# Kernel optimization log

Hardware: AMD Instinct MI355X
Metric: run time of the kernel (lower is better)

Reference implementation:

```python
import jax, jax.numpy as jnp
import numpy as np

N, E = 50000, 1600000
F_IN, EDGE_DIM, HID, HEADS, NCLS = 64, 16, 128, 4, 40
C = HID // HEADS  # per-head dim = 32


def setup_inputs() -> dict:
    key = jax.random.key(0)
    ks = jax.random.split(key, 20)
    s = 0.1
    inp = {
        'x': jax.random.normal(ks[0], (N, F_IN), jnp.float32),
        'edge_index': jax.random.randint(ks[1], (2, E), 0, N, jnp.int64),
        'edge_attr': jax.random.normal(ks[2], (E, EDGE_DIM), jnp.float32),
        # layer 1 params
        'W1': jax.random.normal(ks[3], (HID, F_IN), jnp.float32) * s,
        'as1': jax.random.normal(ks[4], (HEADS, C), jnp.float32) * s,
        'ad1': jax.random.normal(ks[5], (HEADS, C), jnp.float32) * s,
        'ae1': jax.random.normal(ks[6], (HEADS, C), jnp.float32) * s,
        'We1': jax.random.normal(ks[7], (HID, EDGE_DIM), jnp.float32) * s,
        'b1': jnp.zeros((HID,), jnp.float32),
        # layer 2 params
        'W2': jax.random.normal(ks[8], (HID, HID), jnp.float32) * s,
        'as2': jax.random.normal(ks[9], (HEADS, C), jnp.float32) * s,
        'ad2': jax.random.normal(ks[10], (HEADS, C), jnp.float32) * s,
        'ae2': jax.random.normal(ks[11], (HEADS, C), jnp.float32) * s,
        'We2': jax.random.normal(ks[12], (HID, EDGE_DIM), jnp.float32) * s,
        'b2': jnp.zeros((HID,), jnp.float32),
        # final classifier
        'Wlin': jax.random.normal(ks[13], (NCLS, HID), jnp.float32) * s,
        'blin': jnp.zeros((NCLS,), jnp.float32),
    }
    return inp


def gat_conv(x, src, dst, eattr, W, a_s, a_d, a_e, We, b):
    """PyG GATConv (concat=True, add_self_loops=True, fill_value='mean'), eval mode."""
    n = x.shape[0]
    H, Cd = a_s.shape
    h = (x @ W.T).reshape(n, H, Cd)  # [N,H,C]
    # self-loop edge_attr = per-destination mean of incoming edge_attr
    cnt = jax.ops.segment_sum(jnp.ones((dst.shape[0],), eattr.dtype), dst, num_segments=n)
    mean_ea = jax.ops.segment_sum(eattr, dst, num_segments=n) / jnp.maximum(cnt, 1.0)[:, None]
    loops = jnp.arange(n, dtype=src.dtype)
    s_idx = jnp.concatenate([src, loops])
    d_idx = jnp.concatenate([dst, loops])
    ea = jnp.concatenate([eattr, mean_ea], axis=0)  # [E+N, edge_dim]
    e = (ea @ We.T).reshape(-1, H, Cd)
    # edge-wise attention logits
    alpha = (h * a_s).sum(-1)[s_idx] + (h * a_d).sum(-1)[d_idx] + (e * a_e).sum(-1)  # [E+N,H]
    alpha = jax.nn.leaky_relu(alpha, 0.2)
    # segment softmax over destination neighborhoods (every node has a self-loop)
    amax = jax.ops.segment_max(alpha, d_idx, num_segments=n)
    ex = jnp.exp(alpha - amax[d_idx])
    den = jax.ops.segment_sum(ex, d_idx, num_segments=n)
    coef = ex / (den[d_idx] + 1e-16)
    out = jax.ops.segment_sum(h[s_idx] * coef[:, :, None], d_idx, num_segments=n)
    return out.reshape(n, H * Cd) + b


def reference(x, edge_index, edge_attr, W1, as1, ad1, ae1, We1, b1,
              W2, as2, ad2, ae2, We2, b2, Wlin, blin):
    src, dst = edge_index[0], edge_index[1]
    h = jax.nn.relu(gat_conv(x, src, dst, edge_attr, W1, as1, ad1, ae1, We1, b1))
    h = jax.nn.relu(gat_conv(h, src, dst, edge_attr, W2, as2, ad2, ae2, We2, b2))
    logits = h @ Wlin.T + blin
    return jax.nn.log_softmax(logits, axis=1)
```

## Files before the change

kernel.cpp:

```cpp
#include <hip/hip_runtime.h>
#include <hip/hip_bf16.h>
#include <math.h>


#define CHUNK 2048

typedef __attribute__((ext_vector_type(8))) short short8;
typedef __attribute__((ext_vector_type(4))) float floatx4;
typedef __attribute__((ext_vector_type(2))) float floatx2;

__device__ __forceinline__ unsigned short f2bf(float f) {
  unsigned u = __float_as_uint(f);
  unsigned r = u + 0x7FFFu + ((u >> 16) & 1u);
  return (unsigned short)(r >> 16);
}
__device__ __forceinline__ float bf2f(unsigned short b) {
  return __uint_as_float(((unsigned)b) << 16);
}

__global__ __launch_bounds__(128) void wa_kernel(const float* __restrict__ ae1,
                                                 const float* __restrict__ We1,
                                                 const float* __restrict__ ae2,
                                                 const float* __restrict__ We2,
                                                 float* __restrict__ Wa) {
  int t = threadIdx.x;
  const float* ae = (t < 64) ? ae1 : ae2;
  const float* We = (t < 64) ? We1 : We2;
  int h = (t >> 4) & 3;
  int d = t & 15;
  float s = 0.f;
  for (int c = 0; c < 32; ++c) s += ae[h * 32 + c] * We[(h * 32 + c) * 16 + d];
  Wa[t] = s;
}

__global__ __launch_bounds__(256) void alphaseq_kernel(const float* __restrict__ ea,
                                                       const float* __restrict__ Wa,
                                                       uint2* __restrict__ tA1,
                                                       uint2* __restrict__ tA2, int E) {
  __shared__ float wa[128];
  if (threadIdx.x < 128) wa[threadIdx.x] = Wa[threadIdx.x];
  __syncthreads();
  int e = blockIdx.x * 256 + threadIdx.x;
  if (e >= E) return;
  const float4* p = (const float4*)(ea + (size_t)e * 16);
  float4 q0 = p[0], q1 = p[1], q2 = p[2], q3 = p[3];
  float v[16] = {q0.x, q0.y, q0.z, q0.w, q1.x, q1.y, q1.z, q1.w,
                 q2.x, q2.y, q2.z, q2.w, q3.x, q3.y, q3.z, q3.w};
  unsigned short rr[8];
#pragma unroll
  for (int h = 0; h < 8; ++h) {
    float s = 0.f;
#pragma unroll
    for (int d = 0; d < 16; ++d) s += v[d] * wa[h * 16 + d];
    rr[h] = f2bf(s);
  }
  uint2 lo, hi;
  lo.x = ((unsigned)rr[1] << 16) | rr[0];
  lo.y = ((unsigned)rr[3] << 16) | rr[2];
  hi.x = ((unsigned)rr[5] << 16) | rr[4];
  hi.y = ((unsigned)rr[7] << 16) | rr[6];
  tA1[e] = lo;
  tA2[e] = hi;
}

__global__ __launch_bounds__(512) void hist_kernel(const int* __restrict__ dst,
                                                   int* __restrict__ bucketCnt,
                                                   int E, int NB) {
  __shared__ int hist[512];
  const int tid = threadIdx.x;
  hist[tid] = 0;
  __syncthreads();
  const int e0 = blockIdx.x * CHUNK, e1 = min(e0 + CHUNK, E);
  for (int e = e0 + tid; e < e1; e += 512) atomicAdd(&hist[dst[e] >> 7], 1);
  __syncthreads();
  if (tid < NB && hist[tid]) atomicAdd(&bucketCnt[tid], hist[tid]);
}

__global__ __launch_bounds__(512) void scanB_kernel(const int* __restrict__ bucketCnt,
                                                    int* __restrict__ bucketOffs,
                                                    int* __restrict__ bucketPos,
                                                    int* __restrict__ offs,
                                                    int NB, int N, int E) {
  __shared__ int sc[512];
  const int tid = threadIdx.x;
  const int v = (tid < NB) ? bucketCnt[tid] : 0;
  sc[tid] = v;
  __syncthreads();
  for (int off = 1; off < 512; off <<= 1) {
    int t = (tid >= off) ? sc[tid - off] : 0;
    __syncthreads();
    sc[tid] += t;
    __syncthreads();
  }
  const int excl = sc[tid] - v;
  if (tid < NB) { bucketOffs[tid] = excl; bucketPos[tid] = excl; }
  if (tid == 0) { bucketOffs[NB] = E; offs[N] = E; }
}

__global__ __launch_bounds__(512) void partB_kernel(const int* __restrict__ src,
                                                    const int* __restrict__ dst,
                                                    const uint2* __restrict__ tA1,
                                                    const uint2* __restrict__ tA2,
                                                    int* __restrict__ bucketPos,
                                                    int4* __restrict__ binned16,
                                                    int* __restrict__ binned4,
                                                    unsigned char* __restrict__ dlArr,
                                                    int E, int NB) {
  __shared__ int hist[512], sc[512], lbase[513], gbase[512], lcnt[512];
  __shared__ int4 stg16[CHUNK];
  __shared__ int stg4[CHUNK];
  __shared__ unsigned char stg1[CHUNK];
  const int tid = threadIdx.x;
  const int e0 = blockIdx.x * CHUNK;
  const int e1 = min(e0 + CHUNK, E);
  hist[tid] = 0; lcnt[tid] = 0;
  __syncthreads();
  for (int e = e0 + tid; e < e1; e += 512) atomicAdd(&hist[dst[e] >> 7], 1);
  __syncthreads();
  sc[tid] = hist[tid];
  __syncthreads();
  for (int off = 1; off < 512; off <<= 1) {
    int t = (tid >= off) ? sc[tid - off] : 0;
    __syncthreads();
    sc[tid] += t;
    __syncthreads();
  }
  lbase[tid + 1] = sc[tid];
  if (tid == 0) lbase[0] = 0;
  if (tid < NB && hist[tid] > 0) gbase[tid] = atomicAdd(&bucketPos[tid], hist[tid]);
  __syncthreads();
  for (int e = e0 + tid; e < e1; e += 512) {
    const int d = dst[e];
    const int b = d >> 7;
    const int lr = atomicAdd(&lcnt[b], 1);
    const uint2 a1 = tA1[e];
    const uint2 a2 = tA2[e];
    int4 v;
    v.x = (src[e] & 0xFFFF) | ((d & 127) << 16);
    v.y = (int)a1.x;
    v.z = (int)a1.y;
    v.w = (int)a2.x;
    const int sp = lbase[b] + lr;
    stg16[sp] = v;
    stg4[sp] = (int)a2.y;
    stg1[sp] = (unsigned char)(d & 127);
  }
  __syncthreads();
  const int total = e1 - e0;
  for (int t = tid; t < total; t += 512) {
    int lo = 0, hi = 511;
    while (lo < hi) {
      int mid = (lo + hi + 1) >> 1;
      if (lbase[mid] <= t) lo = mid; else hi = mid - 1;
    }
    const int g = gbase[lo] + (t - lbase[lo]);
    binned16[g] = stg16[t];
    binned4[g] = stg4[t];
    dlArr[g] = stg1[t];
  }
}

__global__ __launch_bounds__(256) void passC_kernel(const int4* __restrict__ binned16,
                                                    const int* __restrict__ binned4,
                                                    const unsigned char* __restrict__ dlArr,
                                                    const int* __restrict__ bucketOffs,
                                                    int* __restrict__ srcS,
                                                    uint2* __restrict__ aeS1,
                                                    uint2* __restrict__ aeS2,
                                                    int* __restrict__ offs, int N) {
  __shared__ int cnt[128], dbase[129], dpos[128];
  const int tid = threadIdx.x;
  const int b = blockIdx.x;
  const int bo = bucketOffs[b], be = bucketOffs[b + 1];
  const int m = be - bo;
  if (tid < 128) { cnt[tid] = 0; dpos[tid] = 0; }
  __syncthreads();
  for (int t = tid; t < m; t += 256) atomicAdd(&cnt[dlArr[bo + t]], 1);
  __syncthreads();
  for (int off = 1; off < 128; off <<= 1) {
    int t = (tid < 128 && tid >= (unsigned)off) ? cnt[tid - off] : 0;
    __syncthreads();
    if (tid < 128) cnt[tid] += t;
    __syncthreads();
  }
  if (tid == 0) dbase[0] = 0;
  if (tid < 128) dbase[tid + 1] = cnt[tid];
  __syncthreads();
  const int dcnt = min(128, N - (b << 7));
  if (tid < dcnt) offs[(b << 7) + tid] = bo + dbase[tid];
  for (int t = tid; t < m; t += 256) {
    const int4 v = binned16[bo + t];
    const int w4 = binned4[bo + t];
    const int dl = (v.x >> 16) & 127;
    const int p = dbase[dl] + atomicAdd(&dpos[dl], 1);
    srcS[bo + p] = v.x & 0xFFFF;
    aeS1[bo + p] = make_uint2((unsigned)v.y, (unsigned)v.z);
    aeS2[bo + p] = make_uint2((unsigned)v.w, (unsigned)w4);
  }
}

__global__ __launch_bounds__(256) void cvt2_kernel(const float* __restrict__ a,
                                                   unsigned short* __restrict__ ao, int na,
                                                   const float* __restrict__ b,
                                                   unsigned short* __restrict__ bo, int nb) {
  int i = blockIdx.x * 256 + threadIdx.x;
  if (i < na) ao[i] = f2bf(a[i]);
  else if (i < na + nb) bo[i - na] = f2bf(b[i - na]);
}

__global__ __launch_bounds__(256) void cvtw_kernel(const float* __restrict__ Wlin,
                                                   unsigned short* __restrict__ whi,
                                                   unsigned short* __restrict__ wlo) {
  int i = blockIdx.x * 256 + threadIdx.x;
  if (i >= 48 * 128) return;
  float v = (i < 40 * 128) ? Wlin[i] : 0.f;
  unsigned short h = f2bf(v);
  whi[i] = h;
  wlo[i] = f2bf(v - bf2f(h));
}

__global__ __launch_bounds__(256) void gemm_mfma_f32_kernel(const float* __restrict__ X,
                                                            const unsigned short* __restrict__ Wb,
                                                            unsigned short* __restrict__ H,
                                                            int n) {
  const int w = threadIdx.x >> 6;
  const int lane = threadIdx.x & 63;
  const int m0 = blockIdx.x * 64;
  const int quad = lane >> 4;
  const int l15 = lane & 15;
  floatx4 acc[4][2];
#pragma unroll
  for (int mt = 0; mt < 4; ++mt)
#pragma unroll
    for (int nt = 0; nt < 2; ++nt) acc[mt][nt] = (floatx4)(0.f);

  int rowm[4];
#pragma unroll
  for (int mt = 0; mt < 4; ++mt) {
    int r = m0 + mt * 16 + l15;
    rowm[mt] = (r < n) ? r : (n - 1);
  }
  const int ncol0 = (w << 5) + l15;

#pragma unroll
  for (int kc = 0; kc < 64; kc += 32) {
    const int koff = kc + (quad << 3);
    short8 a[4], b[2];
#pragma unroll
    for (int mt = 0; mt < 4; ++mt) {
      const float* pr = X + (size_t)rowm[mt] * 64 + koff;
      float4 q0 = *(const float4*)pr;
      float4 q1 = *(const float4*)(pr + 4);
      a[mt][0] = (short)f2bf(q0.x); a[mt][1] = (short)f2bf(q0.y);
      a[mt][2] = (short)f2bf(q0.z); a[mt][3] = (short)f2bf(q0.w);
      a[mt][4] = (short)f2bf(q1.x); a[mt][5] = (short)f2bf(q1.y);
      a[mt][6] = (short)f2bf(q1.z); a[mt][7] = (short)f2bf(q1.w);
    }
#pragma unroll
    for (int nt = 0; nt < 2; ++nt)
      b[nt] = *(const short8*)(Wb + (size_t)(ncol0 + nt * 16) * 64 + koff);
#pragma unroll
    for (int mt = 0; mt < 4; ++mt)
#pragma unroll
      for (int nt = 0; nt < 2; ++nt)
        acc[mt][nt] = __builtin_amdgcn_mfma_f32_16x16x32_bf16(a[mt], b[nt], acc[mt][nt], 0, 0, 0);
  }
#pragma unroll
  for (int mt = 0; mt < 4; ++mt) {
    const int rbase = m0 + mt * 16 + (quad << 2);
#pragma unroll
    for (int nt = 0; nt < 2; ++nt) {
      const int col = ncol0 + nt * 16;
#pragma unroll
      for (int r = 0; r < 4; ++r) {
        const int row = rbase + r;
        if (row < n) H[(size_t)row * 128 + col] = f2bf(acc[mt][nt][r]);
      }
    }
  }
}

__global__ __launch_bounds__(256) void gemm_mfma_kernel(const unsigned short* __restrict__ X,
                                                        const unsigned short* __restrict__ Wb,
                                                        unsigned short* __restrict__ H,
                                                        int n, int K) {
  const int w = threadIdx.x >> 6;
  const int lane = threadIdx.x & 63;
  const int m0 = blockIdx.x * 64;
  const int quad = lane >> 4;
  const int l15 = lane & 15;
  floatx4 acc[4][2];
#pragma unroll
  for (int mt = 0; mt < 4; ++mt)
#pragma unroll
    for (int nt = 0; nt < 2; ++nt) acc[mt][nt] = (floatx4)(0.f);

  int rowm[4];
#pragma unroll
  for (int mt = 0; mt < 4; ++mt) {
    int r = m0 + mt * 16 + l15;
    rowm[mt] = (r < n) ? r : (n - 1);
  }
  const int ncol0 = (w << 5) + l15;

  for (int kc = 0; kc < K; kc += 32) {
    const int koff = kc + (quad << 3);
    short8 a[4], b[2];
#pragma unroll
    for (int mt = 0; mt < 4; ++mt)
      a[mt] = *(const short8*)(X + (size_t)rowm[mt] * K + koff);
#pragma unroll
    for (int nt = 0; nt < 2; ++nt)
      b[nt] = *(const short8*)(Wb + (size_t)(ncol0 + nt * 16) * K + koff);
#pragma unroll
    for (int mt = 0; mt < 4; ++mt)
#pragma unroll
      for (int nt = 0; nt < 2; ++nt)
        acc[mt][nt] = __builtin_amdgcn_mfma_f32_16x16x32_bf16(a[mt], b[nt], acc[mt][nt], 0, 0, 0);
  }
#pragma unroll
  for (int mt = 0; mt < 4; ++mt) {
    const int rbase = m0 + mt * 16 + (quad << 2);
#pragma unroll
    for (int nt = 0; nt < 2; ++nt) {
      const int col = ncol0 + nt * 16;
#pragma unroll
      for (int r = 0; r < 4; ++r) {
        const int row = rbase + r;
        if (row < n) H[(size_t)row * 128 + col] = f2bf(acc[mt][nt][r]);
      }
    }
  }
}

__global__ __launch_bounds__(256) void score_kernel(const unsigned short* __restrict__ h,
                                                    const float* __restrict__ a_s,
                                                    const float* __restrict__ a_d,
                                                    float* __restrict__ ssc,
                                                    float* __restrict__ dsc, int n) {
  int gid = blockIdx.x * 256 + threadIdx.x;
  int node = gid >> 6;
  int lane = threadIdx.x & 63;
  if (node >= n) return;
  int ch = lane * 2;
  ushort2 hq = *(const ushort2*)(h + (size_t)node * 128 + ch);
  float h0 = bf2f(hq.x), h1 = bf2f(hq.y);
  float ps = h0 * a_s[ch] + h1 * a_s[ch + 1];
  float pd = h0 * a_d[ch] + h1 * a_d[ch + 1];
#pragma unroll
  for (int off = 8; off; off >>= 1) {
    ps += __shfl_xor(ps, off, 16);
    pd += __shfl_xor(pd, off, 16);
  }
  if ((lane & 15) == 0) {
    int head = lane >> 4;
    ssc[node * 4 + head] = ps;
    dsc[node * 4 + head] = pd;
  }
}

__device__ __forceinline__ float leaky02(float a) { return a > 0.f ? a : 0.2f * a; }
__device__ __forceinline__ float sel4(float4 v, int h) {
  return (h == 0) ? v.x : (h == 1) ? v.y : (h == 2) ? v.z : v.w;
}

__global__ __launch_bounds__(256) void agg_kernel(const unsigned short* __restrict__ hin,
                                                  const float* __restrict__ ssc,
                                                  const float* __restrict__ dsc,
                                                  const unsigned short* __restrict__ aeS,
                                                  const int* __restrict__ offs,
                                                  const int* __restrict__ srcS,
                                                  const float* __restrict__ bias,
                                                  unsigned short* __restrict__ hout, int n) {
  __shared__ int sbuf[4][64];
  __shared__ float pbuf[4][256];
  const int tid = threadIdx.x;
  const int wv = tid >> 6;
  const int lane = tid & 63;
  const int node = blockIdx.x * 4 + wv;
  if (node >= n) return;
  const int l32 = lane & 31;
  const int half = lane >> 5;
  const int ch4 = l32 * 4;
  const int headB = l32 >> 3;
  const float4 dv = *(const float4*)(dsc + (size_t)node * 4);
  float4 l4 = make_float4(0.f, 0.f, 0.f, 0.f);
  float4 sa = make_float4(0.f, 0.f, 0.f, 0.f);
  floatx2 acc01 = (floatx2)(0.f);
  floatx2 acc23 = (floatx2)(0.f);
  const int j0 = offs[node], j1 = offs[node + 1];

  for (int jc = j0; jc < j1; jc += 64) {
    const int len = min(64, j1 - jc);
    float4 p4 = make_float4(0.f, 0.f, 0.f, 0.f);
    int sv = 0;
    if (lane < len) {
      const int j = jc + lane;
      sv = srcS[j];
      const ushort4 aq = *(const ushort4*)(aeS + (size_t)j * 4);
      const float4 ae4 = make_float4(bf2f(aq.x), bf2f(aq.y), bf2f(aq.z), bf2f(aq.w));
      const float4 ss4 = *(const float4*)(ssc + (size_t)sv * 4);
      sa.x += ae4.x; sa.y += ae4.y; sa.z += ae4.z; sa.w += ae4.w;
      p4.x = __expf(leaky02(ss4.x + dv.x + ae4.x));
      p4.y = __expf(leaky02(ss4.y + dv.y + ae4.y));
      p4.z = __expf(leaky02(ss4.z + dv.z + ae4.z));
      p4.w = __expf(leaky02(ss4.w + dv.w + ae4.w));
    }
    sbuf[wv][lane] = sv;
    *(float4*)(&pbuf[wv][lane * 4]) = p4;
    l4.x += p4.x; l4.y += p4.y; l4.z += p4.z; l4.w += p4.w;
    int k = 0;
    for (; k + 8 <= len; k += 8) {
      int s[4];
      float p[4];
      uint2 d[4];
#pragma unroll
      for (int u = 0; u < 4; ++u) {
        const int kk = k + 2 * u + half;
        s[u] = sbuf[wv][kk];
        p[u] = pbuf[wv][kk * 4 + headB];
      }
#pragma unroll
      for (int u = 0; u < 4; ++u)
        d[u] = *(const uint2*)(hin + (size_t)s[u] * 128 + ch4);
#pragma unroll
      for (int u = 0; u < 4; ++u) {
        floatx2 p2; p2.x = p[u]; p2.y = p[u];
        floatx2 h01, h23;
        h01.x = __uint_as_float(d[u].x << 16);
        h01.y = __uint_as_float(d[u].x & 0xFFFF0000u);
        h23.x = __uint_as_float(d[u].y << 16);
        h23.y = __uint_as_float(d[u].y & 0xFFFF0000u);
        acc01 += p2 * h01;
        acc23 += p2 * h23;
      }
    }
    for (; k < len; k += 2) {
      int kk = k + half;
      if (kk < len) {
        int s = sbuf[wv][kk];
        float p = pbuf[wv][kk * 4 + headB];
        uint2 d = *(const uint2*)(hin + (size_t)s * 128 + ch4);
        floatx2 p2; p2.x = p; p2.y = p;
        floatx2 h01, h23;
        h01.x = __uint_as_float(d.x << 16);
        h01.y = __uint_as_float(d.x & 0xFFFF0000u);
        h23.x = __uint_as_float(d.y << 16);
        h23.y = __uint_as_float(d.y & 0xFFFF0000u);
        acc01 += p2 * h01;
        acc23 += p2 * h23;
      }
    }
  }

  float acc[4] = {acc01.x, acc01.y, acc23.x, acc23.y};
#pragma unroll
  for (int off = 32; off; off >>= 1) {
    sa.x += __shfl_xor(sa.x, off);
    sa.y += __shfl_xor(sa.y, off);
    sa.z += __shfl_xor(sa.z, off);
    sa.w += __shfl_xor(sa.w, off);
    l4.x += __shfl_xor(l4.x, off);
    l4.y += __shfl_xor(l4.y, off);
    l4.z += __shfl_xor(l4.z, off);
    l4.w += __shfl_xor(l4.w, off);
  }
#pragma unroll
  for (int i = 0; i < 4; ++i) acc[i] += __shfl_xor(acc[i], 32);

  const int deg = j1 - j0;
  const float invd = 1.f / fmaxf((float)deg, 1.f);
  const float ssn = ssc[(size_t)node * 4 + headB];
  const float aloop = leaky02(ssn + sel4(dv, headB) + sel4(sa, headB) * invd);
  const float pl = __expf(aloop);
  const float lF = sel4(l4, headB) + pl;
  const uint2 hd = *(const uint2*)(hin + (size_t)node * 128 + ch4);
  const float hv0 = __uint_as_float(hd.x << 16);
  const float hv1 = __uint_as_float(hd.x & 0xFFFF0000u);
  const float hv2 = __uint_as_float(hd.y << 16);
  const float hv3 = __uint_as_float(hd.y & 0xFFFF0000u);
  const float inv = 1.f / (lF + 1e-16f);
  const float4 bi = *(const float4*)(bias + ch4);
  const float o0 = fmaxf((acc[0] + pl * hv0) * inv + bi.x, 0.f);
  const float o1 = fmaxf((acc[1] + pl * hv1) * inv + bi.y, 0.f);
  const float o2 = fmaxf((acc[2] + pl * hv2) * inv + bi.z, 0.f);
  const float o3 = fmaxf((acc[3] + pl * hv3) * inv + bi.w, 0.f);
  if (half == 0) {
    ushort4 o;
    o.x = f2bf(o0); o.y = f2bf(o1); o.z = f2bf(o2); o.w = f2bf(o3);
    *(ushort4*)(hout + (size_t)node * 128 + ch4) = o;
  }
}

__global__ __launch_bounds__(256) void classifier_kernel(const unsigned short* __restrict__ h,
                                                         const unsigned short* __restrict__ Whi,
                                                         const unsigned short* __restrict__ Wlo,
                                                         const float* __restrict__ blin,
                                                         float* __restrict__ out, int n) {
  const int w = threadIdx.x >> 6;
  const int lane = threadIdx.x & 63;
  const int quad = lane >> 4;
  const int l15 = lane & 15;
  const int row0 = blockIdx.x * 64 + w * 16;
  if (row0 >= n) return;
  int rowm = row0 + l15;
  if (rowm >= n) rowm = n - 1;
  floatx4 acc[3];
#pragma unroll
  for (int nt = 0; nt < 3; ++nt) acc[nt] = (floatx4)(0.f);
  const size_t hbase = (size_t)rowm * 128;
#pragma unroll
  for (int kc = 0; kc < 128; kc += 32) {
    const int koff = kc + (quad << 3);
    short8 a = *(const short8*)(h + hbase + koff);
#pragma unroll
    for (int nt = 0; nt < 3; ++nt) {
      short8 bh = *(const short8*)(Whi + (size_t)(nt * 16 + l15) * 128 + koff);
      short8 bl = *(const short8*)(Wlo + (size_t)(nt * 16 + l15) * 128 + koff);
      acc[nt] = __builtin_amdgcn_mfma_f32_16x16x32_bf16(a, bh, acc[nt], 0, 0, 0);
      acc[nt] = __builtin_amdgcn_mfma_f32_16x16x32_bf16(a, bl, acc[nt], 0, 0, 0);
    }
  }
  const float bl0 = blin[l15];
  const float bl1 = blin[16 + l15];
  const float bl2 = (l15 < 8) ? blin[32 + l15] : 0.f;
#pragma unroll
  for (int r = 0; r < 4; ++r) {
    const int rrow = row0 + (quad << 2) + r;
    const float v0 = acc[0][r] + bl0;
    const float v1 = acc[1][r] + bl1;
    const float v2 = (l15 < 8) ? (acc[2][r] + bl2) : -INFINITY;
    float m = fmaxf(v0, fmaxf(v1, v2));
#pragma unroll
    for (int off = 8; off; off >>= 1) m = fmaxf(m, __shfl_xor(m, off, 16));
    const float e2 = (l15 < 8) ? __expf(v2 - m) : 0.f;
    float s = __expf(v0 - m) + __expf(v1 - m) + e2;
#pragma unroll
    for (int off = 8; off; off >>= 1) s += __shfl_xor(s, off, 16);
    const float ls = m + __logf(s);
    if (rrow < n) {
      float* po = out + (size_t)rrow * 40;
      po[l15] = v0 - ls;
      po[16 + l15] = v1 - ls;
      if (l15 < 8) po[32 + l15] = v2 - ls;
    }
  }
}

extern "C" void kernel_launch(void* const* d_in, const int* in_sizes, int n_in,
                              void* d_out, int out_size, void* d_ws, size_t ws_size,
                              hipStream_t stream) {
  const float* x    = (const float*)d_in[0];
  const int*   eidx = (const int*)d_in[1];
  const float* ea   = (const float*)d_in[2];
  const float* W1   = (const float*)d_in[3];
  const float* as1  = (const float*)d_in[4];
  const float* ad1  = (const float*)d_in[5];
  const float* ae1w = (const float*)d_in[6];
  const float* We1  = (const float*)d_in[7];
  const float* b1   = (const float*)d_in[8];
  const float* W2   = (const float*)d_in[9];
  const float* as2  = (const float*)d_in[10];
  const float* ad2  = (const float*)d_in[11];
  const float* ae2w = (const float*)d_in[12];
  const float* We2  = (const float*)d_in[13];
  const float* b2   = (const float*)d_in[14];
  const float* Wlin = (const float*)d_in[15];
  const float* blin = (const float*)d_in[16];
  float* out = (float*)d_out;

  const int N = in_sizes[0] / 64;
  const int E = in_sizes[1] / 2;
  const int* src = eidx;
  const int* dst = eidx + E;
  const int NB = (N + 127) >> 7;

  char* wsb = (char*)d_ws;
  size_t off = 0;
  auto alloc = [&](size_t bytes) -> void* {
    void* p = wsb + off;
    off = (off + bytes + 255) & ~(size_t)255;
    return p;
  };
  int* bucketCnt  = (int*)alloc(512 * 4);
  int* bucketOffs = (int*)alloc(513 * 4);
  int* bucketPos  = (int*)alloc(512 * 4);
  int* offs       = (int*)alloc((size_t)(N + 1) * 4);
  uint2* tA1      = (uint2*)alloc((size_t)E * 8);
  uint2* tA2      = (uint2*)alloc((size_t)E * 8);
  void* regC      = alloc((size_t)E * 16);
  int4* binned16  = (int4*)regC;
  unsigned short* hA = (unsigned short*)regC;
  int* binned4    = (int*)alloc((size_t)E * 4);
  unsigned char* dlArr = (unsigned char*)alloc((size_t)E);
  int* srcS       = (int*)alloc((size_t)E * 4);
  float* Wa       = (float*)alloc(128 * 4);
  unsigned short* Wb1 = (unsigned short*)alloc(128 * 64 * 2);
  unsigned short* Wb2 = (unsigned short*)alloc(128 * 128 * 2);
  unsigned short* Wlh = (unsigned short*)alloc(48 * 128 * 2);
  unsigned short* Wll = (unsigned short*)alloc(48 * 128 * 2);
  float* ssc      = (float*)alloc((size_t)N * 4 * 4);
  float* dsc      = (float*)alloc((size_t)N * 4 * 4);
  unsigned short* hB = (unsigned short*)alloc((size_t)N * 128 * 2);
  uint2* aeS1 = tA1;
  uint2* aeS2 = tA2;

  const int ge = (E + 255) / 256;
  const int gg = (N + 63) / 64;
  const int gs = (N + 3) / 4;
  const int gp = (E + CHUNK - 1) / CHUNK;
  const int ncvt = 128 * 64 + 128 * 128;

  hipMemsetAsync(bucketCnt, 0, 512 * 4, stream);
  wa_kernel<<<1, 128, 0, stream>>>(ae1w, We1, ae2w, We2, Wa);
  alphaseq_kernel<<<ge, 256, 0, stream>>>(ea, Wa, tA1, tA2, E);
  hist_kernel<<<gp, 512, 0, stream>>>(dst, bucketCnt, E, NB);
  scanB_kernel<<<1, 512, 0, stream>>>(bucketCnt, bucketOffs, bucketPos, offs, NB, N, E);
  partB_kernel<<<gp, 512, 0, stream>>>(src, dst, tA1, tA2, bucketPos, binned16, binned4,
                                       dlArr, E, NB);
  passC_kernel<<<NB, 256, 0, stream>>>(binned16, binned4, dlArr, bucketOffs, srcS,
                                       aeS1, aeS2, offs, N);

  cvt2_kernel<<<(ncvt + 255) / 256, 256, 0, stream>>>(W1, Wb1, 128 * 64, W2, Wb2, 128 * 128);
  cvtw_kernel<<<24, 256, 0, stream>>>(Wlin, Wlh, Wll);

  gemm_mfma_f32_kernel<<<gg, 256, 0, stream>>>(x, Wb1, hA, N);
  score_kernel<<<gs, 256, 0, stream>>>(hA, as1, ad1, ssc, dsc, N);
  agg_kernel<<<gs, 256, 0, stream>>>(hA, ssc, dsc, (const unsigned short*)aeS1, offs, srcS, b1, hB, N);

  gemm_mfma_kernel<<<gg, 256, 0, stream>>>(hB, Wb2, hA, N, 128);
  score_kernel<<<gs, 256, 0, stream>>>(hA, as2, ad2, ssc, dsc, N);
  agg_kernel<<<gs, 256, 0, stream>>>(hA, ssc, dsc, (const unsigned short*)aeS2, offs, srcS, b2, hB, N);

  classifier_kernel<<<gg, 256, 0, stream>>>(hB, Wlh, Wll, blin, out, N);
}
```

Before: 488.2 us.

## Fuse preprocessing kernels and fold attention scores into GEMM epilogue

Merges wa, alphaseq and histogram into one kernel that computes the edge-attention projection while histogramming destinations. It also combines the three weight conversions into one launch and computes per-head source/destination attention scores in the GEMM epilogue from fp32 accumulators, so the separate score kernels go away. This cuts launches and avoids re-reading the bf16 feature matrix. In exchange each fused block recomputes the small Wa product and runs 256 threads over a 2048-edge chunk, and the scores now come from unrounded accumulators rather than bf16 values.

New measurement: 473.5 us. 3.0% less time.

```diff
diff --git a/kernel.cpp b/kernel.cpp
--- a/kernel.cpp
+++ b/kernel.cpp
@@ -18,62 +18,58 @@
   return __uint_as_float(((unsigned)b) << 16);
 }
 
-__global__ __launch_bounds__(128) void wa_kernel(const float* __restrict__ ae1,
-                                                 const float* __restrict__ We1,
-                                                 const float* __restrict__ ae2,
-                                                 const float* __restrict__ We2,
-                                                 float* __restrict__ Wa) {
-  int t = threadIdx.x;
-  const float* ae = (t < 64) ? ae1 : ae2;
-  const float* We = (t < 64) ? We1 : We2;
-  int h = (t >> 4) & 3;
-  int d = t & 15;
-  float s = 0.f;
-  for (int c = 0; c < 32; ++c) s += ae[h * 32 + c] * We[(h * 32 + c) * 16 + d];
-  Wa[t] = s;
-}
-
 __global__ __launch_bounds__(256) void alphaseq_kernel(const float* __restrict__ ea,
-                                                       const float* __restrict__ Wa,
+                                                       const float* __restrict__ ae1,
+                                                       const float* __restrict__ We1,
+                                                       const float* __restrict__ ae2,
+                                                       const float* __restrict__ We2,
+                                                       const int* __restrict__ dst,
+                                                       int* __restrict__ bucketCnt,
                                                        uint2* __restrict__ tA1,
-                                                       uint2* __restrict__ tA2, int E) {
+                                                       uint2* __restrict__ tA2,
+                                                       int E, int NB) {
   __shared__ float wa[128];
-  if (threadIdx.x < 128) wa[threadIdx.x] = Wa[threadIdx.x];
-  __syncthreads();
-  int e = blockIdx.x * 256 + threadIdx.x;
-  if (e >= E) return;
-  const float4* p = (const float4*)(ea + (size_t)e * 16);
-  float4 q0 = p[0], q1 = p[1], q2 = p[2], q3 = p[3];
-  float v[16] = {q0.x, q0.y, q0.z, q0.w, q1.x, q1.y, q1.z, q1.w,
-                 q2.x, q2.y, q2.z, q2.w, q3.x, q3.y, q3.z, q3.w};
-  unsigned short rr[8];
-#pragma unroll
-  for (int h = 0; h < 8; ++h) {
-    float s = 0.f;
-#pragma unroll
-    for (int d = 0; d < 16; ++d) s += v[d] * wa[h * 16 + d];
-    rr[h] = f2bf(s);
-  }
-  uint2 lo, hi;
-  lo.x = ((unsigned)rr[1] << 16) | rr[0];
-  lo.y = ((unsigned)rr[3] << 16) | rr[2];
-  hi.x = ((unsigned)rr[5] << 16) | rr[4];
-  hi.y = ((unsigned)rr[7] << 16) | rr[6];
-  tA1[e] = lo;
-  tA2[e] = hi;
-}
-
-__global__ __launch_bounds__(512) void hist_kernel(const int* __restrict__ dst,
-                                                   int* __restrict__ bucketCnt,
-                                                   int E, int NB) {
   __shared__ int hist[512];
   const int tid = threadIdx.x;
   hist[tid] = 0;
+  hist[tid + 256] = 0;
+  if (tid < 128) {
+    const float* aev = (tid < 64) ? ae1 : ae2;
+    const float* Wev = (tid < 64) ? We1 : We2;
+    const int h = (tid >> 4) & 3;
+    const int d = tid & 15;
+    float s = 0.f;
+#pragma unroll
+    for (int c = 0; c < 32; ++c) s += aev[h * 32 + c] * Wev[(h * 32 + c) * 16 + d];
+    wa[tid] = s;
+  }
   __syncthreads();
   const int e0 = blockIdx.x * CHUNK, e1 = min(e0 + CHUNK, E);
-  for (int e = e0 + tid; e < e1; e += 512) atomicAdd(&hist[dst[e] >> 7], 1);
-  __syncthreads();
-  if (tid < NB && hist[tid]) atomicAdd(&bucketCnt[tid], hist[tid]);
+  for (int e = e0 + tid; e < e1; e += 256) {
+    atomicAdd(&hist[dst[e] >> 7], 1);
+    const float4* p = (const float4*)(ea + (size_t)e * 16);
+    float4 q0 = p[0], q1 = p[1], q2 = p[2], q3 = p[3];
+    float v[16] = {q0.x, q0.y, q0.z, q0.w, q1.x, q1.y, q1.z, q1.w,
+                   q2.x, q2.y, q2.z, q2.w, q3.x, q3.y, q3.z, q3.w};
+    unsigned short rr[8];
+#pragma unroll
+    for (int h = 0; h < 8; ++h) {
+      float s = 0.f;
+#pragma unroll
+      for (int d = 0; d < 16; ++d) s += v[d] * wa[h * 16 + d];
+      rr[h] = f2bf(s);
+    }
+    uint2 lo, hi;
+    lo.x = ((unsigned)rr[1] << 16) | rr[0];
+    lo.y = ((unsigned)rr[3] << 16) | rr[2];
+    hi.x = ((unsigned)rr[5] << 16) | rr[4];
+    hi.y = ((unsigned)rr[7] << 16) | rr[6];
+    tA1[e] = lo;
+    tA2[e] = hi;
+  }
+  __syncthreads();
+  for (int i = tid; i < NB; i += 256)
+    if (hist[i]) atomicAdd(&bucketCnt[i], hist[i]);
 }
 
 __global__ __launch_bounds__(512) void scanB_kernel(const int* __restrict__ bucketCnt,
@@ -199,30 +195,59 @@
   }
 }
 
-__global__ __launch_bounds__(256) void cvt2_kernel(const float* __restrict__ a,
-                                                   unsigned short* __restrict__ ao, int na,
-                                                   const float* __restrict__ b,
-                                                   unsigned short* __restrict__ bo, int nb) {
+__global__ __launch_bounds__(256) void cvtall_kernel(const float* __restrict__ W1,
+                                                     unsigned short* __restrict__ Wb1,
+                                                     const float* __restrict__ W2,
+                                                     unsigned short* __restrict__ Wb2,
+                                                     const float* __restrict__ Wlin,
+                                                     unsigned short* __restrict__ whi,
+                                                     unsigned short* __restrict__ wlo) {
+  const int n1 = 128 * 64, n2 = 128 * 128, n3 = 48 * 128;
   int i = blockIdx.x * 256 + threadIdx.x;
-  if (i < na) ao[i] = f2bf(a[i]);
-  else if (i < na + nb) bo[i - na] = f2bf(b[i - na]);
-}
-
-__global__ __launch_bounds__(256) void cvtw_kernel(const float* __restrict__ Wlin,
-                                                   unsigned short* __restrict__ whi,
-                                                   unsigned short* __restrict__ wlo) {
-  int i = blockIdx.x * 256 + threadIdx.x;
-  if (i >= 48 * 128) return;
-  float v = (i < 40 * 128) ? Wlin[i] : 0.f;
-  unsigned short h = f2bf(v);
-  whi[i] = h;
-  wlo[i] = f2bf(v - bf2f(h));
-}
-
-__global__ __launch_bounds__(256) void gemm_mfma_f32_kernel(const float* __restrict__ X,
-                                                            const unsigned short* __restrict__ Wb,
-                                                            unsigned short* __restrict__ H,
-                                                            int n) {
+  if (i < n1) {
+    Wb1[i] = f2bf(W1[i]);
+  } else if (i < n1 + n2) {
+    Wb2[i - n1] = f2bf(W2[i - n1]);
+  } else if (i < n1 + n2 + n3) {
+    const int j = i - n1 - n2;
+    float v = (j < 40 * 128) ? Wlin[j] : 0.f;
+    unsigned short h = f2bf(v);
+    whi[j] = h;
+    wlo[j] = f2bf(v - bf2f(h));
+  }
+}
+
+#define GEMM_SCORE_EPILOGUE()                                                      \
+  {                                                                                \
+    const float as0 = a_s[ncol0], as1v = a_s[ncol0 + 16];                          \
+    const float ad0 = a_d[ncol0], ad1v = a_d[ncol0 + 16];                          \
+    _Pragma("unroll") for (int mt = 0; mt < 4; ++mt) {                             \
+      _Pragma("unroll") for (int r = 0; r < 4; ++r) {                              \
+        float ps = acc[mt][0][r] * as0 + acc[mt][1][r] * as1v;                     \
+        float pd = acc[mt][0][r] * ad0 + acc[mt][1][r] * ad1v;                     \
+        _Pragma("unroll") for (int off = 8; off; off >>= 1) {                      \
+          ps += __shfl_xor(ps, off, 16);                                           \
+          pd += __shfl_xor(pd, off, 16);                                           \
+        }                                                                          \
+        if (l15 == 0) {                                                            \
+          const int row = m0 + mt * 16 + (quad << 2) + r;                          \
+          if (row < n) {                                                           \
+            ssc[(size_t)row * 4 + w] = ps;                                         \
+            dsc[(size_t)row * 4 + w] = pd;                                         \
+          }                                                                        \
+        }                                                                          \
+      }                                                                            \
+    }                                                                              \
+  }
+
+__global__ __launch_bounds__(256) void gemm_score_f32_kernel(const float* __restrict__ X,
+                                                             const unsigned short* __restrict__ Wb,
+                                                             const float* __restrict__ a_s,
+                                                             const float* __restrict__ a_d,
+                                                             unsigned short* __restrict__ H,
+                                                             float* __restrict__ ssc,
+                                                             float* __restrict__ dsc,
+                                                             int n) {
   const int w = threadIdx.x >> 6;
   const int lane = threadIdx.x & 63;
   const int m0 = blockIdx.x * 64;
@@ -278,12 +303,17 @@
       }
     }
   }
-}
-
-__global__ __launch_bounds__(256) void gemm_mfma_kernel(const unsigned short* __restrict__ X,
-                                                        const unsigned short* __restrict__ Wb,
-                                                        unsigned short* __restrict__ H,
-                                                        int n, int K) {
+  GEMM_SCORE_EPILOGUE()
+}
+
+__global__ __launch_bounds__(256) void gemm_score_kernel(const unsigned short* __restrict__ X,
+                                                         const unsigned short* __restrict__ Wb,
+                                                         const float* __restrict__ a_s,
+                                                         const float* __restrict__ a_d,
+                                                         unsigned short* __restrict__ H,
+                                                         float* __restrict__ ssc,
+                                                         float* __restrict__ dsc,
+                                                         int n, int K) {
   const int w = threadIdx.x >> 6;
   const int lane = threadIdx.x & 63;
   const int m0 = blockIdx.x * 64;
@@ -331,32 +361,7 @@
       }
     }
   }
-}
-
-__global__ __launch_bounds__(256) void score_kernel(const unsigned short* __restrict__ h,
-                                                    const float* __restrict__ a_s,
-                                                    const float* __restrict__ a_d,
-                                                    float* __restrict__ ssc,
-                                                    float* __restrict__ dsc, int n) {
-  int gid = blockIdx.x * 256 + threadIdx.x;
-  int node = gid >> 6;
-  int lane = threadIdx.x & 63;
-  if (node >= n) return;
-  int ch = lane * 2;
-  ushort2 hq = *(const ushort2*)(h + (size_t)node * 128 + ch);
-  float h0 = bf2f(hq.x), h1 = bf2f(hq.y);
-  float ps = h0 * a_s[ch] + h1 * a_s[ch + 1];
-  float pd = h0 * a_d[ch] + h1 * a_d[ch + 1];
-#pragma unroll
-  for (int off = 8; off; off >>= 1) {
-    ps += __shfl_xor(ps, off, 16);
-    pd += __shfl_xor(pd, off, 16);
-  }
-  if ((lane & 15) == 0) {
-    int head = lane >> 4;
-    ssc[node * 4 + head] = ps;
-    dsc[node * 4 + head] = pd;
-  }
+  GEMM_SCORE_EPILOGUE()
 }
 
 __device__ __forceinline__ float leaky02(float a) { return a > 0.f ? a : 0.2f * a; }
@@ -594,7 +599,6 @@
   int* binned4    = (int*)alloc((size_t)E * 4);
   unsigned char* dlArr = (unsigned char*)alloc((size_t)E);
   int* srcS       = (int*)alloc((size_t)E * 4);
-  float* Wa       = (float*)alloc(128 * 4);
   unsigned short* Wb1 = (unsigned short*)alloc(128 * 64 * 2);
   unsigned short* Wb2 = (unsigned short*)alloc(128 * 128 * 2);
   unsigned short* Wlh = (unsigned short*)alloc(48 * 128 * 2);
@@ -605,31 +609,26 @@
   uint2* aeS1 = tA1;
   uint2* aeS2 = tA2;
 
-  const int ge = (E + 255) / 256;
   const int gg = (N + 63) / 64;
   const int gs = (N + 3) / 4;
   const int gp = (E + CHUNK - 1) / CHUNK;
-  const int ncvt = 128 * 64 + 128 * 128;
+  const int ncvt = 128 * 64 + 128 * 128 + 48 * 128;
 
   hipMemsetAsync(bucketCnt, 0, 512 * 4, stream);
-  wa_kernel<<<1, 128, 0, stream>>>(ae1w, We1, ae2w, We2, Wa);
-  alphaseq_kernel<<<ge, 256, 0, stream>>>(ea, Wa, tA1, tA2, E);
-  hist_kernel<<<gp, 512, 0, stream>>>(dst, bucketCnt, E, NB);
+  alphaseq_kernel<<<gp, 256, 0, stream>>>(ea, ae1w, We1, ae2w, We2, dst, bucketCnt,
+                                          tA1, tA2, E, NB);
   scanB_kernel<<<1, 512, 0, stream>>>(bucketCnt, bucketOffs, bucketPos, offs, NB, N, E);
   partB_kernel<<<gp, 512, 0, stream>>>(src, dst, tA1, tA2, bucketPos, binned16, binned4,
                                        dlArr, E, NB);
   passC_kernel<<<NB, 256, 0, stream>>>(binned16, binned4, dlArr, bucketOffs, srcS,
                                        aeS1, aeS2, offs, N);
 
-  cvt2_kernel<<<(ncvt + 255) / 256, 256, 0, stream>>>(W1, Wb1, 128 * 64, W2, Wb2, 128 * 128);
-  cvtw_kernel<<<24, 256, 0, stream>>>(Wlin, Wlh, Wll);
-
-  gemm_mfma_f32_kernel<<<gg, 256, 0, stream>>>(x, Wb1, hA, N);
-  score_kernel<<<gs, 256, 0, stream>>>(hA, as1, ad1, ssc, dsc, N);
+  cvtall_kernel<<<(ncvt + 255) / 256, 256, 0, stream>>>(W1, Wb1, W2, Wb2, Wlin, Wlh, Wll);
+
+  gemm_score_f32_kernel<<<gg, 256, 0, stream>>>(x, Wb1, as1, ad1, hA, ssc, dsc, N);
   agg_kernel<<<gs, 256, 0, stream>>>(hA, ssc, dsc, (const unsigned short*)aeS1, offs, srcS, b1, hB, N);
 
-  gemm_mfma_kernel<<<gg, 256, 0, stream>>>(hB, Wb2, hA, N, 128);
-  score_kernel<<<gs, 256, 0, stream>>>(hA, as2, ad2, ssc, dsc, N);
+  gemm_score_kernel<<<gg, 256, 0, stream>>>(hB, Wb2, as2, ad2, hA, ssc, dsc, N, 128);
   agg_kernel<<<gs, 256, 0, stream>>>(hA, ssc, dsc, (const unsigned short*)aeS2, offs, srcS, b2, hB, N);
 
   classifier_kernel<<<gg, 256, 0, stream>>>(hB, Wlh, Wll, blin, out, N);
```
